# Kernel optimization log

Hardware: AMD Instinct MI355X
Metric: run time of the kernel (lower is better)

## Reference

```python
import jax, jax.numpy as jnp
import numpy as np

B, IN, F, HID, D, RH, OUT, C, R = 4096, 1024, 512, 128, 128, 64, 1, 10, 16


def setup_inputs() -> dict:
    key = jax.random.key(0)
    ks = jax.random.split(key, 24)
    def p(k, shape, s=0.05):
        return jax.random.normal(k, shape, jnp.float32) * s
    return {
        'x': jax.random.normal(ks[0], (B, IN), jnp.float32),
        'pref': jax.random.uniform(ks[1], (R, 2), jnp.float32),
        'base_w': p(ks[2], (F, IN)), 'base_b': p(ks[3], (F,)),
        'wm1_w': p(ks[4], (16, 2)), 'wm1_b': p(ks[5], (16,)),
        'wm2_w': p(ks[6], (C, 16)), 'wm2_b': p(ks[7], (C,)),
        'ray0_w': p(ks[8], (C, RH, 2)), 'ray0_b': p(ks[9], (C, RH)),
        'ray2_w': p(ks[10], (C, D, RH)), 'ray2_b': p(ks[11], (C, D)),
        'fc1_w': p(ks[12], (C, HID * F, D)), 'fc1_b': p(ks[13], (C, HID * F)),
        'b1_w': p(ks[14], (C, HID, D)), 'b1_b': p(ks[15], (C, HID)),
        'fc2_w': p(ks[16], (C, OUT * HID, D)), 'fc2_b': p(ks[17], (C, OUT * HID)),
        'b2_w': p(ks[18], (C, OUT, D)), 'b2_b': p(ks[19], (C, OUT)),
    }


def reference(x, pref, base_w, base_b, wm1_w, wm1_b, wm2_w, wm2_b,
              ray0_w, ray0_b, ray2_w, ray2_b, fc1_w, fc1_b,
              b1_w, b1_b, fc2_w, fc2_b, b2_w, b2_b):
    # base feature extractor: (B, F)
    feature = x @ base_w.T + base_b
    # client mixing weights per ray: (R, C), normalized over clients
    h = jax.nn.relu(pref @ wm1_w.T + wm1_b)
    w = jax.nn.sigmoid(h @ wm2_w.T + wm2_b)
    w = w / jnp.sum(w, axis=1, keepdims=True)
    # merged ray-MLP (nonlinear -> merge the tiny weights explicitly per ray)
    m0w = jnp.einsum('rc,cod->rod', w, ray0_w)          # (R, RH, 2)
    r1 = jax.nn.relu(jnp.einsum('rd,rod->ro', pref, m0w) + w @ ray0_b)
    m2w = jnp.einsum('rc,coh->roh', w, ray2_w)          # (R, D, RH)
    ray2v = jnp.einsum('rh,roh->ro', r1, m2w) + w @ ray2_b  # (R, D)

    def hyper(Wc, bc):
        # sum_c w[r,c] * (ray2v[r] @ Wc[c].T + bc[c])  == F.linear with merged params
        per_client = jnp.einsum('rd,cod->rco', ray2v, Wc)   # (R, C, O)
        return jnp.einsum('rc,rco->ro', w, per_client) + w @ bc

    W1 = hyper(fc1_w, fc1_b).reshape(R, HID, F)   # generated layer-1 weight
    b1 = hyper(b1_w, b1_b)                        # (R, HID)
    W2 = hyper(fc2_w, fc2_b).reshape(R, OUT, HID) # generated layer-2 weight
    b2 = hyper(b2_w, b2_b)                        # (R, OUT)

    v1 = jnp.einsum('bf,rhf->rbh', feature, W1) + b1[:, None, :]  # (R, B, HID)
    out = jnp.einsum('rbh,roh->rbo', v1, W2) + b2[:, None, :]     # (R, B, OUT)
    return jax.nn.sigmoid(out), out
```

## Files before the change

### kernel.cpp

```cpp
#include <hip/hip_runtime.h>
#include <hip/hip_cooperative_groups.h>
#include <cstddef>
#include <cstdint>


#define WS_WT    0
#define WS_RV    160
#define WS_W2T   2208
#define WS_WEFF  4256
#define WS_WFIN  12448
#define WS_BFIN  28832
#define WS_ZERO_BEG WS_RV
#define WS_ZERO_CNT (WS_BFIN + 16 - WS_RV)

namespace cg = cooperative_groups;

__device__ __forceinline__ void front_mlp_flat(const float* __restrict__ pref,
                                               const float* __restrict__ wm1_w,
                                               const float* __restrict__ wm1_b,
                                               const float* __restrict__ wm2_w,
                                               const float* __restrict__ wm2_b,
                                               float* sh1, float* sw, float* sinv) {
  const int t = threadIdx.x;
  {
    int r = t >> 4, j = t & 15;
    float v = pref[r * 2 + 0] * wm1_w[j * 2 + 0] + pref[r * 2 + 1] * wm1_w[j * 2 + 1] + wm1_b[j];
    sh1[r * 16 + j] = fmaxf(v, 0.f);
  }
  __syncthreads();
  if (t < 160) {
    int r = t / 10, c = t % 10;
    float z = wm2_b[c];
    for (int j = 0; j < 16; ++j) z += sh1[r * 16 + j] * wm2_w[c * 16 + j];
    sw[r * 10 + c] = 1.f / (1.f + expf(-z));
  }
  __syncthreads();
  if (t < 16) {
    float s = 0.f;
    for (int c = 0; c < 10; ++c) s += sw[t * 10 + c];
    sinv[t] = 1.f / s;
  }
  __syncthreads();
  if (t < 160) {
    int r = t / 10, c = t % 10;
    sw[r * 10 + c] = sw[r * 10 + c] * sinv[r];
  }
  __syncthreads();
}

__global__ __launch_bounds__(256, 2) void k_all(
    const float* __restrict__ x, const float* __restrict__ pref,
    const float* __restrict__ base_w, const float* __restrict__ base_b,
    const float* __restrict__ wm1_w, const float* __restrict__ wm1_b,
    const float* __restrict__ wm2_w, const float* __restrict__ wm2_b,
    const float* __restrict__ ray0_w, const float* __restrict__ ray0_b,
    const float* __restrict__ ray2_w, const float* __restrict__ ray2_b,
    const float* __restrict__ fc1_w, const float* __restrict__ fc1_b,
    const float* __restrict__ b1_w, const float* __restrict__ b1_b,
    const float* __restrict__ fc2_w, const float* __restrict__ fc2_b,
    const float* __restrict__ b2_w, const float* __restrict__ b2_b,
    float* __restrict__ ws, float* __restrict__ out) {
  __shared__ float4 sm4[4096];
  float* smf = (float*)sm4;
  cg::grid_group grid = cg::this_grid();
  const int t = threadIdx.x;
  const int blk = blockIdx.x;
  const int gid = blk * 256 + t;

  if (gid < 12288) ws[WS_RV + gid] = 0.f;
  else if (gid < 12304) ws[WS_BFIN + (gid - 12288)] = 0.f;
  grid.sync();

  if (blk < 80) {
    float* sh1  = smf;
    float* sw   = smf + 256;
    float* sinv = smf + 416;
    float* r1s  = smf + 432;
    front_mlp_flat(pref, wm1_w, wm1_b, wm2_w, wm2_b, sh1, sw, sinv);
    for (int it = t; it < 1024; it += 256) {
      int r = it >> 6, o = it & 63;
      float m0 = 0.f, m1 = 0.f, rb = 0.f;
      for (int c = 0; c < 10; ++c) {
        float wv = sw[r * 10 + c];
        m0 += wv * ray0_w[(c * 64 + o) * 2 + 0];
        m1 += wv * ray0_w[(c * 64 + o) * 2 + 1];
        rb += wv * ray0_b[c * 64 + o];
      }
      float v = pref[r * 2 + 0] * m0 + pref[r * 2 + 1] * m1 + rb;
      r1s[r * 65 + o] = fmaxf(v, 0.f);
    }
    __syncthreads();
    const int pair = blk * 16 + (t >> 4);
    const int r = t & 15;
    const float* row = ray2_w + (size_t)pair * 64;
    const float* r1r = r1s + r * 65;
    float dot = 0.f;
#pragma unroll
    for (int k = 0; k < 64; ++k) dot += row[k] * r1r[k];
    int c = pair >> 7, d = pair & 127;
    atomicAdd(&ws[WS_RV + r * 128 + d], sw[r * 10 + c] * dot);

    if (blk == 0) {
      if (t < 160) ws[WS_WT + t] = sw[(t & 15) * 10 + (t >> 4)];
      for (int i = t; i < 2048; i += 256) {
        int rr = i >> 7, dd = i & 127;
        float s = 0.f;
        for (int cc = 0; cc < 10; ++cc) s += sw[rr * 10 + cc] * ray2_b[cc * 128 + dd];
        atomicAdd(&ws[WS_RV + i], s);
      }
    } else if (blk == 1) {
      for (int i = t; i < 2048; i += 256) {
        int h = i >> 4, rr = i & 15;
        float s = 0.f;
        for (int cc = 0; cc < 10; ++cc) s += sw[rr * 10 + cc] * fc2_b[cc * 128 + h];
        atomicAdd(&ws[WS_W2T + i], s);
      }
    }
  }
  grid.sync();

  {
    const int wid = t >> 6, lane = t & 63;
    const int rid = blk * 4 + wid;
    if (rid < 1280) {
      float2 rvl[16];
#pragma unroll
      for (int r = 0; r < 16; ++r) rvl[r] = *(const float2*)&ws[WS_RV + r * 128 + lane * 2];
      float2 a = *(const float2*)&fc2_w[(size_t)rid * 128 + lane * 2];
      float u[16];
#pragma unroll
      for (int r = 0; r < 16; ++r) u[r] = a.x * rvl[r].x + a.y * rvl[r].y;
#pragma unroll
      for (int m = 1; m <= 32; m <<= 1) {
#pragma unroll
        for (int r = 0; r < 16; ++r) u[r] += __shfl_xor(u[r], m, 64);
      }
      if (lane == 0) {
        int c = rid >> 7, h = rid & 127;
#pragma unroll
        for (int r = 0; r < 16; ++r)
          atomicAdd(&ws[WS_W2T + h * 16 + r], u[r] * ws[WS_WT + c * 16 + r]);
      }
    }
  }
  grid.sync();

  {
    float* scoef = smf;
    float* bfred = smf + 2560;
    const int wid = t >> 6, lane = t & 63, l32 = lane & 31;
    const int ch0 = (blk >> 6) * 160;
    const int fp  = (blk & 63) * 4 + wid;
    for (int i = t; i < 2560; i += 256) {
      int chl = i >> 4, r = i & 15;
      int ch = ch0 + chl, c = ch >> 7, h = ch & 127;
      scoef[i] = ws[WS_WT + c * 16 + r] * ws[WS_W2T + h * 16 + r];
    }
    float4 rv[16];
#pragma unroll
    for (int r = 0; r < 16; ++r) rv[r] = *(const float4*)&ws[WS_RV + r * 128 + l32 * 4];
    __syncthreads();

    float acc[16];
#pragma unroll
    for (int r = 0; r < 16; ++r) acc[r] = 0.f;

    const float4* p = (const float4*)fc1_w + (size_t)ch0 * 16384 + fp * 64 + lane;
    float4 buf[8];
#pragma unroll
    for (int j = 0; j < 8; ++j) buf[j] = p[(size_t)j * 16384];

    for (int g = 0; g < 20; ++g) {
#pragma unroll
      for (int k = 0; k < 8; ++k) {
        const int chl = g * 8 + k;
        float4 cur = buf[k];
        int nxt = chl + 8; if (nxt > 159) nxt = 159;
        buf[k] = p[(size_t)nxt * 16384];
        const float4* cf = (const float4*)(scoef + chl * 16);
        float4 c0 = cf[0], c1 = cf[1], c2 = cf[2], c3 = cf[3];
        float cw[16] = {c0.x, c0.y, c0.z, c0.w, c1.x, c1.y, c1.z, c1.w,
                        c2.x, c2.y, c2.z, c2.w, c3.x, c3.y, c3.z, c3.w};
#pragma unroll
        for (int r = 0; r < 16; ++r) {
          float tt = cur.x * rv[r].x + cur.y * rv[r].y + cur.z * rv[r].z + cur.w * rv[r].w;
          acc[r] = fmaf(cw[r], tt, acc[r]);
        }
      }
    }
#pragma unroll
    for (int m = 1; m <= 16; m <<= 1) {
#pragma unroll
      for (int r = 0; r < 16; ++r) acc[r] += __shfl_xor(acc[r], m, 64);
    }
    if (l32 == 0) {
      const int f = fp * 2 + (lane >> 5);
#pragma unroll
      for (int r = 0; r < 16; ++r) atomicAdd(&ws[WS_WEFF + r * 512 + f], acc[r]);
    }
    __syncthreads();

    if (blk < 16) {
      const int bb = blk;
      const int f = (bb & 1) * 256 + t;
      const int ch0b = (bb >> 1) * 160;
      for (int i = t; i < 2560; i += 256) {
        int chl = i >> 4, r = i & 15;
        int ch = ch0b + chl, c = ch >> 7, h = ch & 127;
        scoef[i] = ws[WS_WT + c * 16 + r] * ws[WS_W2T + h * 16 + r];
      }
      __syncthreads();
      float a2[16];
#pragma unroll
      for (int r = 0; r < 16; ++r) a2[r] = 0.f;
      const float* q = fc1_b + (size_t)ch0b * 512 + f;
      float b4[4];
#pragma unroll
      for (int j = 0; j < 4; ++j) b4[j] = q[(size_t)j * 512];
      for (int g = 0; g < 40; ++g) {
#pragma unroll
        for (int k = 0; k < 4; ++k) {
          const int it = g * 4 + k;
          float xv = b4[k];
          int nxt = it + 4; if (nxt > 159) nxt = 159;
          b4[k] = q[(size_t)nxt * 512];
          const float4* cf = (const float4*)(scoef + it * 16);
          float4 c0 = cf[0], c1 = cf[1], c2 = cf[2], c3 = cf[3];
          float cw[16] = {c0.x, c0.y, c0.z, c0.w, c1.x, c1.y, c1.z, c1.w,
                          c2.x, c2.y, c2.z, c2.w, c3.x, c3.y, c3.z, c3.w};
#pragma unroll
          for (int r = 0; r < 16; ++r) a2[r] = fmaf(cw[r], xv, a2[r]);
        }
      }
#pragma unroll
      for (int r = 0; r < 16; ++r) atomicAdd(&ws[WS_WEFF + r * 512 + f], a2[r]);
    } else if (blk < 24) {
      const int hb = blk - 16;
      const int ch0b = hb * 160;
      for (int i = t; i < 2560; i += 256) {
        int chl = i >> 4, r = i & 15;
        int ch = ch0b + chl, c = ch >> 7, h = ch & 127;
        scoef[i] = ws[WS_WT + c * 16 + r] * ws[WS_W2T + h * 16 + r];
      }
      __syncthreads();
      float2 rv2[16];
#pragma unroll
      for (int r = 0; r < 16; ++r) rv2[r] = *(const float2*)&ws[WS_RV + r * 128 + lane * 2];
      float a2[16];
#pragma unroll
      for (int r = 0; r < 16; ++r) a2[r] = 0.f;
      const int chl0 = wid * 40;
      const float2* q = (const float2*)b1_w + (size_t)(ch0b + chl0) * 64 + lane;
      float2 b2buf[4];
#pragma unroll
      for (int j = 0; j < 4; ++j) b2buf[j] = q[(size_t)j * 64];
      for (int g = 0; g < 10; ++g) {
#pragma unroll
        for (int k = 0; k < 4; ++k) {
          const int it = g * 4 + k;
          float2 cur = b2buf[k];
          int nxt = it + 4; if (nxt > 39) nxt = 39;
          b2buf[k] = q[(size_t)nxt * 64];
          const float4* cf = (const float4*)(scoef + (chl0 + it) * 16);
          float4 c0 = cf[0], c1 = cf[1], c2 = cf[2], c3 = cf[3];
          float cw[16] = {c0.x, c0.y, c0.z, c0.w, c1.x, c1.y, c1.z, c1.w,
                          c2.x, c2.y, c2.z, c2.w, c3.x, c3.y, c3.z, c3.w};
#pragma unroll
          for (int r = 0; r < 16; ++r)
            a2[r] = fmaf(cw[r], cur.x * rv2[r].x + cur.y * rv2[r].y, a2[r]);
        }
      }
#pragma unroll
      for (int m = 1; m <= 32; m <<= 1) {
#pragma unroll
        for (int r = 0; r < 16; ++r) a2[r] += __shfl_xor(a2[r], m, 64);
      }
      if (lane == 0) {
#pragma unroll
        for (int r = 0; r < 16; ++r) bfred[wid * 16 + r] = a2[r];
      }
      __syncthreads();
      if (t < 16)
        atomicAdd(&ws[WS_BFIN + t], bfred[t] + bfred[16 + t] + bfred[32 + t] + bfred[48 + t]);
    } else if (blk == 24) {
      float a2[16];
#pragma unroll
      for (int r = 0; r < 16; ++r) a2[r] = 0.f;
      for (int i = t; i < 1280; i += 256) {
        int c = i >> 7, h = i & 127;
        float v = b1_b[c * 128 + h];
#pragma unroll
        for (int r = 0; r < 16; ++r)
          a2[r] = fmaf(ws[WS_WT + c * 16 + r] * ws[WS_W2T + h * 16 + r], v, a2[r]);
      }
      for (int i = t; i < 1280; i += 256) {
        int c = i >> 7, d = i & 127;
        float v = b2_w[c * 128 + d];
#pragma unroll
        for (int r = 0; r < 16; ++r)
          a2[r] = fmaf(ws[WS_WT + c * 16 + r] * ws[WS_RV + r * 128 + d], v, a2[r]);
      }
      if (t < 10) {
        float v = b2_b[t];
#pragma unroll
        for (int r = 0; r < 16; ++r) a2[r] = fmaf(ws[WS_WT + t * 16 + r], v, a2[r]);
      }
#pragma unroll
      for (int m = 1; m <= 32; m <<= 1) {
#pragma unroll
        for (int r = 0; r < 16; ++r) a2[r] += __shfl_xor(a2[r], m, 64);
      }
      if (lane == 0) {
#pragma unroll
        for (int r = 0; r < 16; ++r) bfred[wid * 16 + r] = a2[r];
      }
      __syncthreads();
      if (t < 16)
        atomicAdd(&ws[WS_BFIN + t], bfred[t] + bfred[16 + t] + bfred[32 + t] + bfred[48 + t]);
    }
  }
  grid.sync();

  if (blk < 32) {
    const int il = t & 31, fg = t >> 5;
    const int i = blk * 32 + il;
    const float* WEFF = ws + WS_WEFF;
    float a4[16];
#pragma unroll
    for (int r = 0; r < 16; ++r) a4[r] = 0.f;
    const int f0 = fg * 64;
    for (int f = f0; f < f0 + 64; ++f) {
      float bw = base_w[(size_t)f * 1024 + i];
#pragma unroll
      for (int r = 0; r < 16; ++r) a4[r] = fmaf(WEFF[r * 512 + f], bw, a4[r]);
    }
    float* red = smf;
#pragma unroll
    for (int r = 0; r < 16; ++r) red[fg * 512 + il * 16 + r] = a4[r];
    __syncthreads();
    for (int o = t; o < 512; o += 256) {
      int ir = o >> 4, r = o & 15;
      float s = 0.f;
#pragma unroll
      for (int fg2 = 0; fg2 < 8; ++fg2) s += red[fg2 * 512 + ir * 16 + r];
      ws[WS_WFIN + r * 1024 + blk * 32 + ir] = s;
    }
  } else if (blk == 32) {
    if (t < 64) {
      const float* WEFF = ws + WS_WEFF;
      float a2[16];
#pragma unroll
      for (int r = 0; r < 16; ++r) a2[r] = 0.f;
      for (int f = t; f < 512; f += 64) {
        float v = base_b[f];
#pragma unroll
        for (int r = 0; r < 16; ++r) a2[r] = fmaf(WEFF[r * 512 + f], v, a2[r]);
      }
#pragma unroll
      for (int m = 1; m <= 32; m <<= 1) {
#pragma unroll
        for (int r = 0; r < 16; ++r) a2[r] += __shfl_xor(a2[r], m, 64);
      }
      if (t == 0) {
#pragma unroll
        for (int r = 0; r < 16; ++r) atomicAdd(&ws[WS_BFIN + r], a2[r]);
      }
    }
  }
  grid.sync();

  if (blk < 256) {
    float4* wfs = sm4;
    const float4* wf4 = (const float4*)(ws + WS_WFIN);
#pragma unroll
    for (int k = 0; k < 16; ++k) wfs[t + 256 * k] = wf4[t + 256 * k];
    __syncthreads();

    const int b0 = blk * 16;
    const int bp = t >> 5;
    const int isub = t & 31;
    const int bA = b0 + bp * 2;
    const float* xa = x + (size_t)bA * 1024;
    const float* xb = xa + 1024;
    float acc0[16], acc1[16];
#pragma unroll
    for (int r = 0; r < 16; ++r) { acc0[r] = 0.f; acc1[r] = 0.f; }

    for (int chunk = 0; chunk < 4; ++chunk) {
#pragma unroll
      for (int j = 0; j < 2; ++j) {
        const int off = chunk * 256 + j * 128 + isub * 4;
        float4 xv0 = *(const float4*)&xa[off];
        float4 xv1 = *(const float4*)&xb[off];
        const float4* wrow = wfs + chunk * 64 + j * 32 + isub;
#pragma unroll
        for (int r = 0; r < 16; ++r) {
          float4 w = wrow[r * 256];
          acc0[r] += xv0.x * w.x + xv0.y * w.y + xv0.z * w.z + xv0.w * w.w;
          acc1[r] += xv1.x * w.x + xv1.y * w.y + xv1.z * w.z + xv1.w * w.w;
        }
      }
    }
#pragma unroll
    for (int m = 1; m <= 16; m <<= 1) {
#pragma unroll
      for (int r = 0; r < 16; ++r) {
        acc0[r] += __shfl_xor(acc0[r], m, 64);
        acc1[r] += __shfl_xor(acc1[r], m, 64);
      }
    }
    if (isub == 0) {
#pragma unroll
      for (int r = 0; r < 16; ++r) {
        float bf = ws[WS_BFIN + r];
        float v0 = acc0[r] + bf;
        float v1 = acc1[r] + bf;
        out[r * 4096 + bA] = 1.f / (1.f + expf(-v0));
        out[r * 4096 + bA + 1] = 1.f / (1.f + expf(-v1));
        out[65536 + r * 4096 + bA] = v0;
        out[65536 + r * 4096 + bA + 1] = v1;
      }
    }
  }
}

__device__ __forceinline__ void front_mlp(const float* __restrict__ pref,
                                          const float* __restrict__ wm1_w,
                                          const float* __restrict__ wm1_b,
                                          const float* __restrict__ wm2_w,
                                          const float* __restrict__ wm2_b,
                                          float (*sh1)[16], float (*sw)[10],
                                          float* sinv) {
  const int t = threadIdx.x;
  {
    int r = t >> 4, j = t & 15;
    float v = pref[r * 2 + 0] * wm1_w[j * 2 + 0] + pref[r * 2 + 1] * wm1_w[j * 2 + 1] + wm1_b[j];
    sh1[r][j] = fmaxf(v, 0.f);
  }
  __syncthreads();
  if (t < 160) {
    int r = t / 10, c = t % 10;
    float z = wm2_b[c];
    for (int j = 0; j < 16; ++j) z += sh1[r][j] * wm2_w[c * 16 + j];
    sw[r][c] = 1.f / (1.f + expf(-z));
  }
  __syncthreads();
  if (t < 16) {
    float s = 0.f;
    for (int c = 0; c < 10; ++c) s += sw[t][c];
    sinv[t] = 1.f / s;
  }
  __syncthreads();
  if (t < 160) {
    int r = t / 10, c = t % 10;
    sw[r][c] = sw[r][c] * sinv[r];
  }
  __syncthreads();
}

__global__ __launch_bounds__(256) void k_stage1(
    const float* __restrict__ pref, const float* __restrict__ wm1_w,
    const float* __restrict__ wm1_b, const float* __restrict__ wm2_w,
    const float* __restrict__ wm2_b, const float* __restrict__ ray0_w,
    const float* __restrict__ ray0_b, const float* __restrict__ ray2_w,
    const float* __restrict__ ray2_b, const float* __restrict__ fc2_b,
    float* __restrict__ ws) {
  __shared__ float sh1[16][16];
  __shared__ float sw[16][10];
  __shared__ float sinv[16];
  __shared__ float r1s[16][65];
  const int t = threadIdx.x;
  front_mlp(pref, wm1_w, wm1_b, wm2_w, wm2_b, sh1, sw, sinv);
  for (int it = t; it < 1024; it += 256) {
    int r = it >> 6, o = it & 63;
    float m0 = 0.f, m1 = 0.f, rb = 0.f;
    for (int c = 0; c < 10; ++c) {
      float wv = sw[r][c];
      m0 += wv * ray0_w[(c * 64 + o) * 2 + 0];
      m1 += wv * ray0_w[(c * 64 + o) * 2 + 1];
      rb += wv * ray0_b[c * 64 + o];
    }
    float v = pref[r * 2 + 0] * m0 + pref[r * 2 + 1] * m1 + rb;
    r1s[r][o] = fmaxf(v, 0.f);
  }
  __syncthreads();
  const int pair = blockIdx.x * 16 + (t >> 4);
  const int r = t & 15;
  const float* row = ray2_w + (size_t)pair * 64;
  const float* r1r = r1s[r];
  float dot = 0.f;
#pragma unroll
  for (int k = 0; k < 64; ++k) dot += row[k] * r1r[k];
  int c = pair >> 7, d = pair & 127;
  atomicAdd(&ws[WS_RV + r * 128 + d], sw[r][c] * dot);

  if (blockIdx.x == 0) {
    if (t < 160) ws[WS_WT + t] = sw[t & 15][t >> 4];
    for (int i = t; i < 2048; i += 256) {
      int rr = i >> 7, dd = i & 127;
      float s = 0.f;
      for (int cc = 0; cc < 10; ++cc) s += sw[rr][cc] * ray2_b[cc * 128 + dd];
      atomicAdd(&ws[WS_RV + i], s);
    }
  } else if (blockIdx.x == 1) {
    for (int i = t; i < 2048; i += 256) {
      int h = i >> 4, rr = i & 15;
      float s = 0.f;
      for (int cc = 0; cc < 10; ++cc) s += sw[rr][cc] * fc2_b[cc * 128 + h];
      atomicAdd(&ws[WS_W2T + i], s);
    }
  }
}

__global__ __launch_bounds__(256) void k_stage2(const float* __restrict__ fc2_w,
                                                float* __restrict__ ws) {
  const int t = threadIdx.x;
  const int lane = t & 63;
  const int wv = blockIdx.x * 4 + (t >> 6);
  float2 rv2[16];
#pragma unroll
  for (int r = 0; r < 16; ++r) rv2[r] = *(const float2*)&ws[WS_RV + r * 128 + lane * 2];
  for (int q = 0; q < 4; ++q) {
    int rid = wv * 4 + q;
    int c = rid >> 7, h = rid & 127;
    float2 a = *(const float2*)&fc2_w[(size_t)rid * 128 + lane * 2];
    float u[16];
#pragma unroll
    for (int r = 0; r < 16; ++r) u[r] = a.x * rv2[r].x + a.y * rv2[r].y;
#pragma unroll
    for (int m = 1; m <= 32; m <<= 1) {
#pragma unroll
      for (int r = 0; r < 16; ++r) u[r] += __shfl_xor(u[r], m, 64);
    }
    if (lane == 0) {
#pragma unroll
      for (int r = 0; r < 16; ++r)
        atomicAdd(&ws[WS_W2T + h * 16 + r], u[r] * ws[WS_WT + c * 16 + r]);
    }
  }
}

__global__ __launch_bounds__(256, 3) void k_main(
    const float* __restrict__ fc1_w, const float* __restrict__ fc1_b,
    const float* __restrict__ b1_w, const float* __restrict__ b1_b,
    const float* __restrict__ b2_w, const float* __restrict__ b2_b,
    float* __restrict__ ws) {
  __shared__ float scoef[2560];
  __shared__ float bfred[4][16];
  const int blk = blockIdx.x;
  const int t = threadIdx.x;

  if (blk < 2048) {
    const int wid = t >> 6, lane = t & 63, l32 = lane & 31;
    const int ch0 = (blk >> 6) * 40;
    const int fp = (blk & 63) * 4 + wid;
    for (int i = t; i < 640; i += 256) {
      int chl = i >> 4, r = i & 15;
      int ch = ch0 + chl, c = ch >> 7, h = ch & 127;
      scoef[i] = ws[WS_WT + c * 16 + r] * ws[WS_W2T + h * 16 + r];
    }
    float4 rv[16];
#pragma unroll
    for (int r = 0; r < 16; ++r) rv[r] = *(const float4*)&ws[WS_RV + r * 128 + l32 * 4];
    __syncthreads();

    float acc[16];
#pragma unroll
    for (int r = 0; r < 16; ++r) acc[r] = 0.f;

    const float4* p = (const float4*)fc1_w + (size_t)ch0 * 16384 + fp * 64 + lane;

    float4 buf[8];
#pragma unroll
    for (int j = 0; j < 8; ++j) buf[j] = p[(size_t)j * 16384];

    for (int g = 0; g < 5; ++g) {
#pragma unroll
      for (int k = 0; k < 8; ++k) {
        const int chl = g * 8 + k;
        float4 cur = buf[k];
        int nxt = chl + 8; if (nxt > 39) nxt = 39;
        buf[k] = p[(size_t)nxt * 16384];
        const float4* cf = (const float4*)(scoef + chl * 16);
        float4 c0 = cf[0], c1 = cf[1], c2 = cf[2], c3 = cf[3];
        float cw[16] = {c0.x, c0.y, c0.z, c0.w, c1.x, c1.y, c1.z, c1.w,
                        c2.x, c2.y, c2.z, c2.w, c3.x, c3.y, c3.z, c3.w};
#pragma unroll
        for (int r = 0; r < 16; ++r) {
          float tt = cur.x * rv[r].x + cur.y * rv[r].y + cur.z * rv[r].z + cur.w * rv[r].w;
          acc[r] = fmaf(cw[r], tt, acc[r]);
        }
      }
    }

#pragma unroll
    for (int m = 1; m <= 16; m <<= 1) {
#pragma unroll
      for (int r = 0; r < 16; ++r) acc[r] += __shfl_xor(acc[r], m, 64);
    }
    if (l32 == 0) {
      const int f = fp * 2 + (lane >> 5);
#pragma unroll
      for (int r = 0; r < 16; ++r) atomicAdd(&ws[WS_WEFF + r * 512 + f], acc[r]);
    }
  } else if (blk < 2064) {
    const int bb = blk - 2048;
    const int f = (bb & 1) * 256 + t;
    const int ch0 = (bb >> 1) * 160;
    for (int i = t; i < 2560; i += 256) {
      int chl = i >> 4, r = i & 15;
      int ch = ch0 + chl, c = ch >> 7, h = ch & 127;
      scoef[i] = ws[WS_WT + c * 16 + r] * ws[WS_W2T + h * 16 + r];
    }
    __syncthreads();
    float acc[16];
#pragma unroll
    for (int r = 0; r < 16; ++r) acc[r] = 0.f;
    const float* q = fc1_b + (size_t)ch0 * 512 + f;
    float b4[4];
#pragma unroll
    for (int j = 0; j < 4; ++j) b4[j] = q[(size_t)j * 512];
    for (int g = 0; g < 40; ++g) {
#pragma unroll
      for (int k = 0; k < 4; ++k) {
        const int it = g * 4 + k;
        float xv = b4[k];
        int nxt = it + 4; if (nxt > 159) nxt = 159;
        b4[k] = q[(size_t)nxt * 512];
        const float4* cf = (const float4*)(scoef + it * 16);
        float4 c0 = cf[0], c1 = cf[1], c2 = cf[2], c3 = cf[3];
        float cw[16] = {c0.x, c0.y, c0.z, c0.w, c1.x, c1.y, c1.z, c1.w,
                        c2.x, c2.y, c2.z, c2.w, c3.x, c3.y, c3.z, c3.w};
#pragma unroll
        for (int r = 0; r < 16; ++r) acc[r] = fmaf(cw[r], xv, acc[r]);
      }
    }
#pragma unroll
    for (int r = 0; r < 16; ++r) atomicAdd(&ws[WS_WEFF + r * 512 + f], acc[r]);
  } else if (blk < 2072) {
    const int hb = blk - 2064;
    const int wid = t >> 6, lane = t & 63;
    const int ch0b = hb * 160;
    for (int i = t; i < 2560; i += 256) {
      int chl = i >> 4, r = i & 15;
      int ch = ch0b + chl, c = ch >> 7, h = ch & 127;
      scoef[i] = ws[WS_WT + c * 16 + r] * ws[WS_W2T + h * 16 + r];
    }
    __syncthreads();
    float2 rv2[16];
#pragma unroll
    for (int r = 0; r < 16; ++r) rv2[r] = *(const float2*)&ws[WS_RV + r * 128 + lane * 2];
    float acc[16];
#pragma unroll
    for (int r = 0; r < 16; ++r) acc[r] = 0.f;
    const int chl0 = wid * 40;
    const float2* q = (const float2*)b1_w + (size_t)(ch0b + chl0) * 64 + lane;
    float2 b2buf[4];
#pragma unroll
    for (int j = 0; j < 4; ++j) b2buf[j] = q[(size_t)j * 64];
    for (int g = 0; g < 10; ++g) {
#pragma unroll
      for (int k = 0; k < 4; ++k) {
        const int it = g * 4 + k;
        float2 cur = b2buf[k];
        int nxt = it + 4; if (nxt > 39) nxt = 39;
        b2buf[k] = q[(size_t)nxt * 64];
        const float4* cf = (const float4*)(scoef + (chl0 + it) * 16);
        float4 c0 = cf[0], c1 = cf[1], c2 = cf[2], c3 = cf[3];
        float cw[16] = {c0.x, c0.y, c0.z, c0.w, c1.x, c1.y, c1.z, c1.w,
                        c2.x, c2.y, c2.z, c2.w, c3.x, c3.y, c3.z, c3.w};
#pragma unroll
        for (int r = 0; r < 16; ++r)
          acc[r] = fmaf(cw[r], cur.x * rv2[r].x + cur.y * rv2[r].y, acc[r]);
      }
    }
#pragma unroll
    for (int m = 1; m <= 32; m <<= 1) {
#pragma unroll
      for (int r = 0; r < 16; ++r) acc[r] += __shfl_xor(acc[r], m, 64);
    }
    if (lane == 0) {
#pragma unroll
      for (int r = 0; r < 16; ++r) bfred[wid][r] = acc[r];
    }
    __syncthreads();
    if (t < 16)
      atomicAdd(&ws[WS_BFIN + t], bfred[0][t] + bfred[1][t] + bfred[2][t] + bfred[3][t]);
  } else {
    const int wid = t >> 6, lane = t & 63;
    float acc[16];
#pragma unroll
    for (int r = 0; r < 16; ++r) acc[r] = 0.f;
    for (int i = t; i < 1280; i += 256) {
      int c = i >> 7, h = i & 127;
      float v = b1_b[c * 128 + h];
#pragma unroll
      for (int r = 0; r < 16; ++r)
        acc[r] = fmaf(ws[WS_WT + c * 16 + r] * ws[WS_W2T + h * 16 + r], v, acc[r]);
    }
    for (int i = t; i < 1280; i += 256) {
      int c = i >> 7, d = i & 127;
      float v = b2_w[c * 128 + d];
#pragma unroll
      for (int r = 0; r < 16; ++r)
        acc[r] = fmaf(ws[WS_WT + c * 16 + r] * ws[WS_RV + r * 128 + d], v, acc[r]);
    }
    if (t < 10) {
      float v = b2_b[t];
#pragma unroll
      for (int r = 0; r < 16; ++r) acc[r] = fmaf(ws[WS_WT + t * 16 + r], v, acc[r]);
    }
#pragma unroll
    for (int m = 1; m <= 32; m <<= 1) {
#pragma unroll
      for (int r = 0; r < 16; ++r) acc[r] += __shfl_xor(acc[r], m, 64);
    }
    if (lane == 0) {
#pragma unroll
      for (int r = 0; r < 16; ++r) bfred[wid][r] = acc[r];
    }
    __syncthreads();
    if (t < 16)
      atomicAdd(&ws[WS_BFIN + t], bfred[0][t] + bfred[1][t] + bfred[2][t] + bfred[3][t]);
  }
}

__global__ __launch_bounds__(256) void k_wfin(const float* __restrict__ base_w,
                                              const float* __restrict__ base_b,
                                              float* __restrict__ ws) {
  const int t = threadIdx.x;
  const int blk = blockIdx.x;
  const int i = (blk & 3) * 256 + t;
  const int f0 = (blk >> 2) * 16;
  const float* WEFF = ws + WS_WEFF;
  float acc[16];
#pragma unroll
  for (int r = 0; r < 16; ++r) acc[r] = 0.f;
#pragma unroll 4
  for (int f = f0; f < f0 + 16; ++f) {
    float bw = base_w[(size_t)f * 1024 + i];
#pragma unroll
    for (int r = 0; r < 16; ++r) acc[r] = fmaf(WEFF[r * 512 + f], bw, acc[r]);
  }
#pragma unroll
  for (int r = 0; r < 16; ++r) atomicAdd(&ws[WS_WFIN + r * 1024 + i], acc[r]);

  if (blk == 0 && t < 64) {
    float a2[16];
#pragma unroll
    for (int r = 0; r < 16; ++r) a2[r] = 0.f;
    for (int f = t; f < 512; f += 64) {
      float v = base_b[f];
#pragma unroll
      for (int r = 0; r < 16; ++r) a2[r] = fmaf(WEFF[r * 512 + f], v, a2[r]);
    }
#pragma unroll
    for (int m = 1; m <= 32; m <<= 1) {
#pragma unroll
      for (int r = 0; r < 16; ++r) a2[r] += __shfl_xor(a2[r], m, 64);
    }
    if (t == 0) {
#pragma unroll
      for (int r = 0; r < 16; ++r) atomicAdd(&ws[WS_BFIN + r], a2[r]);
    }
  }
}

__global__ __launch_bounds__(256) void k_out(const float* __restrict__ x,
                                             const float* __restrict__ ws,
                                             float* __restrict__ out) {
  __shared__ float4 wfs[4096];
  const int t = threadIdx.x;
  const float4* wf4 = (const float4*)(ws + WS_WFIN);
#pragma unroll
  for (int k = 0; k < 16; ++k) wfs[t + 256 * k] = wf4[t + 256 * k];
  __syncthreads();

  const int b0 = blockIdx.x * 16;
  const int bp = t >> 5;
  const int isub = t & 31;
  const int bA = b0 + bp * 2;
  const float* xa = x + (size_t)bA * 1024;
  const float* xb = xa + 1024;
  float acc0[16], acc1[16];
#pragma unroll
  for (int r = 0; r < 16; ++r) { acc0[r] = 0.f; acc1[r] = 0.f; }

  for (int chunk = 0; chunk < 4; ++chunk) {
#pragma unroll
    for (int j = 0; j < 2; ++j) {
      const int off = chunk * 256 + j * 128 + isub * 4;
      float4 xv0 = *(const float4*)&xa[off];
      float4 xv1 = *(const float4*)&xb[off];
      const float4* wrow = wfs + chunk * 64 + j * 32 + isub;
#pragma unroll
      for (int r = 0; r < 16; ++r) {
        float4 w = wrow[r * 256];
        acc0[r] += xv0.x * w.x + xv0.y * w.y + xv0.z * w.z + xv0.w * w.w;
        acc1[r] += xv1.x * w.x + xv1.y * w.y + xv1.z * w.z + xv1.w * w.w;
      }
    }
  }
#pragma unroll
  for (int m = 1; m <= 16; m <<= 1) {
#pragma unroll
    for (int r = 0; r < 16; ++r) {
      acc0[r] += __shfl_xor(acc0[r], m, 64);
      acc1[r] += __shfl_xor(acc1[r], m, 64);
    }
  }
  if (isub == 0) {
#pragma unroll
    for (int r = 0; r < 16; ++r) {
      float bf = ws[WS_BFIN + r];
      float v0 = acc0[r] + bf;
      float v1 = acc1[r] + bf;
      out[r * 4096 + bA] = 1.f / (1.f + expf(-v0));
      out[r * 4096 + bA + 1] = 1.f / (1.f + expf(-v1));
      out[65536 + r * 4096 + bA] = v0;
      out[65536 + r * 4096 + bA + 1] = v1;
    }
  }
}

extern "C" void kernel_launch(void* const* d_in, const int* in_sizes, int n_in,
                              void* d_out, int out_size, void* d_ws, size_t ws_size,
                              hipStream_t stream) {
  (void)in_sizes; (void)n_in; (void)out_size; (void)ws_size;
  const float* x      = (const float*)d_in[0];
  const float* pref   = (const float*)d_in[1];
  const float* base_w = (const float*)d_in[2];
  const float* base_b = (const float*)d_in[3];
  const float* wm1_w  = (const float*)d_in[4];
  const float* wm1_b  = (const float*)d_in[5];
  const float* wm2_w  = (const float*)d_in[6];
  const float* wm2_b  = (const float*)d_in[7];
  const float* ray0_w = (const float*)d_in[8];
  const float* ray0_b = (const float*)d_in[9];
  const float* ray2_w = (const float*)d_in[10];
  const float* ray2_b = (const float*)d_in[11];
  const float* fc1_w  = (const float*)d_in[12];
  const float* fc1_b  = (const float*)d_in[13];
  const float* b1_w   = (const float*)d_in[14];
  const float* b1_b   = (const float*)d_in[15];
  const float* fc2_w  = (const float*)d_in[16];
  const float* fc2_b  = (const float*)d_in[17];
  const float* b2_w   = (const float*)d_in[18];
  const float* b2_b   = (const float*)d_in[19];
  float* ws  = (float*)d_ws;
  float* out = (float*)d_out;

  static int g_mode = -1;
  if (g_mode < 0) {
    int maxb = 0;
    hipError_t e1 = hipOccupancyMaxActiveBlocksPerMultiprocessor(&maxb, k_all, 256, 0);
    int coop = 0, dev = 0;
    (void)hipGetDevice(&dev);
    hipError_t e2 = hipDeviceGetAttribute(&coop, hipDeviceAttributeCooperativeLaunch, dev);
    g_mode = (e1 == hipSuccess && maxb >= 2 && (e2 != hipSuccess || coop != 0)) ? 1 : 0;
  }

  if (g_mode == 1) {
    void* args[] = {
        (void*)&x, (void*)&pref, (void*)&base_w, (void*)&base_b,
        (void*)&wm1_w, (void*)&wm1_b, (void*)&wm2_w, (void*)&wm2_b,
        (void*)&ray0_w, (void*)&ray0_b, (void*)&ray2_w, (void*)&ray2_b,
        (void*)&fc1_w, (void*)&fc1_b, (void*)&b1_w, (void*)&b1_b,
        (void*)&fc2_w, (void*)&fc2_b, (void*)&b2_w, (void*)&b2_b,
        (void*)&ws, (void*)&out};
    hipError_t e = hipLaunchCooperativeKernel(k_all, dim3(512), dim3(256), args, 0, stream);
    if (e == hipSuccess) return;
    g_mode = 0;
  }

  hipMemsetAsync(ws + WS_ZERO_BEG, 0, (size_t)WS_ZERO_CNT * sizeof(float), stream);
  k_stage1<<<80, 256, 0, stream>>>(pref, wm1_w, wm1_b, wm2_w, wm2_b,
                                   ray0_w, ray0_b, ray2_w, ray2_b, fc2_b, ws);
  k_stage2<<<80, 256, 0, stream>>>(fc2_w, ws);
  k_main<<<2073, 256, 0, stream>>>(fc1_w, fc1_b, b1_w, b1_b, b2_w, b2_b, ws);
  k_wfin<<<128, 256, 0, stream>>>(base_w, base_b, ws);
  k_out<<<256, 256, 0, stream>>>(x, ws, out);
}
```

Baseline: 557.9 us.

## Recompute small ray-MLP stages per block to drop grid syncs and atomics

Every block now redundantly computes the mixing weights, the merged ray vector and the generated layer-2 weights in shared memory. This removes the initial zero-fill pass and two grid-wide barriers along with their atomic accumulations. Per-slice partial sums for the effective weights and the final bias are written to separate workspace slots and reduced by the consumers, so no atomics are needed. The fc1 bias contribution is folded into the main fc1 pass. The cost is redundant per-block compute on fc2_w and ray2_w (each block reads all of fc2_w) and extra partial-sum traffic.

```diff
diff --git a/kernel.cpp b/kernel.cpp
--- a/kernel.cpp
+++ b/kernel.cpp
@@ -3,6 +3,10 @@
 #include <cstddef>
 #include <cstdint>
 
+
+#define WS2_WEFFP 0
+#define WS2_WFIN  65536
+#define WS2_PARTS 81920
 
 #define WS_WT    0
 #define WS_RV    160
@@ -61,22 +65,25 @@
     const float* __restrict__ b2_w, const float* __restrict__ b2_b,
     float* __restrict__ ws, float* __restrict__ out) {
   __shared__ float4 sm4[4096];
+  __shared__ float bfin_s[16];
   float* smf = (float*)sm4;
+  float* sw   = smf;
+  float* sinv = smf + 160;
+  float* sh1  = smf + 176;
+  float* rvl  = smf + 432;
+  float* w2t  = smf + 2544;
+  float* X    = smf + 4720;
+  float* bfred= smf + 8880;
+
   cg::grid_group grid = cg::this_grid();
   const int t = threadIdx.x;
   const int blk = blockIdx.x;
-  const int gid = blk * 256 + t;
-
-  if (gid < 12288) ws[WS_RV + gid] = 0.f;
-  else if (gid < 12304) ws[WS_BFIN + (gid - 12288)] = 0.f;
-  grid.sync();
-
-  if (blk < 80) {
-    float* sh1  = smf;
-    float* sw   = smf + 256;
-    float* sinv = smf + 416;
-    float* r1s  = smf + 432;
-    front_mlp_flat(pref, wm1_w, wm1_b, wm2_w, wm2_b, sh1, sw, sinv);
+  const int wid = t >> 6, lane = t & 63, l32 = lane & 31;
+
+  front_mlp_flat(pref, wm1_w, wm1_b, wm2_w, wm2_b, sh1, sw, sinv);
+
+  {
+    float* r1s = X;
     for (int it = t; it < 1024; it += 256) {
       int r = it >> 6, o = it & 63;
       float m0 = 0.f, m1 = 0.f, rb = 0.f;
@@ -90,86 +97,103 @@
       r1s[r * 65 + o] = fmaxf(v, 0.f);
     }
     __syncthreads();
-    const int pair = blk * 16 + (t >> 4);
-    const int r = t & 15;
-    const float* row = ray2_w + (size_t)pair * 64;
-    const float* r1r = r1s + r * 65;
-    float dot = 0.f;
-#pragma unroll
-    for (int k = 0; k < 64; ++k) dot += row[k] * r1r[k];
-    int c = pair >> 7, d = pair & 127;
-    atomicAdd(&ws[WS_RV + r * 128 + d], sw[r * 10 + c] * dot);
-
-    if (blk == 0) {
-      if (t < 160) ws[WS_WT + t] = sw[(t & 15) * 10 + (t >> 4)];
-      for (int i = t; i < 2048; i += 256) {
-        int rr = i >> 7, dd = i & 127;
-        float s = 0.f;
-        for (int cc = 0; cc < 10; ++cc) s += sw[rr * 10 + cc] * ray2_b[cc * 128 + dd];
-        atomicAdd(&ws[WS_RV + i], s);
-      }
-    } else if (blk == 1) {
-      for (int i = t; i < 2048; i += 256) {
-        int h = i >> 4, rr = i & 15;
-        float s = 0.f;
-        for (int cc = 0; cc < 10; ++cc) s += sw[rr * 10 + cc] * fc2_b[cc * 128 + h];
-        atomicAdd(&ws[WS_W2T + i], s);
-      }
-    }
-  }
-  grid.sync();
+    const int d = t & 127, rh = (t >> 7) * 8;
+    float accv[8];
+#pragma unroll
+    for (int j = 0; j < 8; ++j) accv[j] = 0.f;
+    for (int c = 0; c < 10; ++c) {
+      const float4* row4 = (const float4*)(ray2_w + (size_t)(c * 128 + d) * 64);
+      float dtmp[8];
+#pragma unroll
+      for (int j = 0; j < 8; ++j) dtmp[j] = 0.f;
+#pragma unroll
+      for (int k4 = 0; k4 < 16; ++k4) {
+        float4 rw = row4[k4];
+#pragma unroll
+        for (int rr = 0; rr < 8; ++rr) {
+          const float* rr1 = r1s + (rh + rr) * 65 + k4 * 4;
+          dtmp[rr] += rw.x * rr1[0] + rw.y * rr1[1] + rw.z * rr1[2] + rw.w * rr1[3];
+        }
+      }
+      float rb = ray2_b[c * 128 + d];
+#pragma unroll
+      for (int rr = 0; rr < 8; ++rr)
+        accv[rr] += sw[(rh + rr) * 10 + c] * (dtmp[rr] + rb);
+    }
+#pragma unroll
+    for (int rr = 0; rr < 8; ++rr) rvl[(rh + rr) * 132 + d] = accv[rr];
+  }
+  __syncthreads();
 
   {
-    const int wid = t >> 6, lane = t & 63;
-    const int rid = blk * 4 + wid;
-    if (rid < 1280) {
-      float2 rvl[16];
-#pragma unroll
-      for (int r = 0; r < 16; ++r) rvl[r] = *(const float2*)&ws[WS_RV + r * 128 + lane * 2];
-      float2 a = *(const float2*)&fc2_w[(size_t)rid * 128 + lane * 2];
-      float u[16];
-#pragma unroll
-      for (int r = 0; r < 16; ++r) u[r] = a.x * rvl[r].x + a.y * rvl[r].y;
-#pragma unroll
-      for (int m = 1; m <= 32; m <<= 1) {
-#pragma unroll
-        for (int r = 0; r < 16; ++r) u[r] += __shfl_xor(u[r], m, 64);
-      }
-      if (lane == 0) {
-        int c = rid >> 7, h = rid & 127;
-#pragma unroll
-        for (int r = 0; r < 16; ++r)
-          atomicAdd(&ws[WS_W2T + h * 16 + r], u[r] * ws[WS_WT + c * 16 + r]);
-      }
-    }
-  }
-  grid.sync();
+    float* stg = X;
+    const int hl = t >> 3;
+    const int rg = (t & 7) * 2;
+    float accw[4][2];
+#pragma unroll
+    for (int a = 0; a < 4; ++a) { accw[a][0] = 0.f; accw[a][1] = 0.f; }
+    for (int c = 0; c < 10; ++c) {
+      for (int ch = 0; ch < 4; ++ch) {
+        __syncthreads();
+        const float4* src = (const float4*)(fc2_w + ((size_t)c * 128 + ch * 32) * 128);
+#pragma unroll
+        for (int k = 0; k < 4; ++k) {
+          int j = t + 256 * k;
+          int h_loc = j >> 5, dof = (j & 31) * 4;
+          float4 v = src[j];
+          float* dst = stg + h_loc * 130 + dof;
+          ((float2*)dst)[0] = make_float2(v.x, v.y);
+          ((float2*)dst)[1] = make_float2(v.z, v.w);
+        }
+        __syncthreads();
+        float dt0 = 0.f, dt1 = 0.f;
+        const float2* srow = (const float2*)(stg + hl * 130);
+        const float2* rv0 = (const float2*)(rvl + (rg + 0) * 132);
+        const float2* rv1 = (const float2*)(rvl + (rg + 1) * 132);
+#pragma unroll 8
+        for (int d2 = 0; d2 < 64; ++d2) {
+          float2 fv = srow[d2];
+          float2 a0 = rv0[d2], a1 = rv1[d2];
+          dt0 += fv.x * a0.x + fv.y * a0.y;
+          dt1 += fv.x * a1.x + fv.y * a1.y;
+        }
+        int h = ch * 32 + hl;
+        float fb = fc2_b[c * 128 + h];
+        accw[ch][0] += sw[(rg + 0) * 10 + c] * (dt0 + fb);
+        accw[ch][1] += sw[(rg + 1) * 10 + c] * (dt1 + fb);
+      }
+    }
+#pragma unroll
+    for (int ch = 0; ch < 4; ++ch) {
+      int h = ch * 32 + hl;
+      w2t[h * 17 + rg] = accw[ch][0];
+      w2t[h * 17 + rg + 1] = accw[ch][1];
+    }
+  }
+  __syncthreads();
+
+  float* scoef = X;
+  const int cc = blk >> 6;
+  const int ch0 = cc * 160;
+  const int fp = (blk & 63) * 4 + wid;
+  for (int i = t; i < 2560; i += 256) {
+    int chl = i >> 4, r = i & 15;
+    int ch = ch0 + chl;
+    scoef[i] = sw[r * 10 + (ch >> 7)] * w2t[(ch & 127) * 17 + r];
+  }
+  float4 rv[16];
+#pragma unroll
+  for (int r = 0; r < 16; ++r) rv[r] = *(const float4*)&rvl[r * 132 + l32 * 4];
+  __syncthreads();
 
   {
-    float* scoef = smf;
-    float* bfred = smf + 2560;
-    const int wid = t >> 6, lane = t & 63, l32 = lane & 31;
-    const int ch0 = (blk >> 6) * 160;
-    const int fp  = (blk & 63) * 4 + wid;
-    for (int i = t; i < 2560; i += 256) {
-      int chl = i >> 4, r = i & 15;
-      int ch = ch0 + chl, c = ch >> 7, h = ch & 127;
-      scoef[i] = ws[WS_WT + c * 16 + r] * ws[WS_W2T + h * 16 + r];
-    }
-    float4 rv[16];
-#pragma unroll
-    for (int r = 0; r < 16; ++r) rv[r] = *(const float4*)&ws[WS_RV + r * 128 + l32 * 4];
-    __syncthreads();
-
     float acc[16];
 #pragma unroll
     for (int r = 0; r < 16; ++r) acc[r] = 0.f;
-
     const float4* p = (const float4*)fc1_w + (size_t)ch0 * 16384 + fp * 64 + lane;
     float4 buf[8];
 #pragma unroll
     for (int j = 0; j < 8; ++j) buf[j] = p[(size_t)j * 16384];
-
     for (int g = 0; g < 20; ++g) {
 #pragma unroll
       for (int k = 0; k < 8; ++k) {
@@ -188,143 +212,124 @@
         }
       }
     }
+    const int f = fp * 2 + (lane >> 5);
+#pragma unroll
+    for (int j = 0; j < 5; ++j) {
+      int chl = l32 + j * 32;
+      float fb = fc1_b[(size_t)(ch0 + chl) * 512 + f];
+#pragma unroll
+      for (int r = 0; r < 16; ++r) acc[r] = fmaf(scoef[chl * 16 + r], fb, acc[r]);
+    }
 #pragma unroll
     for (int m = 1; m <= 16; m <<= 1) {
 #pragma unroll
       for (int r = 0; r < 16; ++r) acc[r] += __shfl_xor(acc[r], m, 64);
     }
     if (l32 == 0) {
-      const int f = fp * 2 + (lane >> 5);
-#pragma unroll
-      for (int r = 0; r < 16; ++r) atomicAdd(&ws[WS_WEFF + r * 512 + f], acc[r]);
-    }
-    __syncthreads();
-
-    if (blk < 16) {
-      const int bb = blk;
-      const int f = (bb & 1) * 256 + t;
-      const int ch0b = (bb >> 1) * 160;
-      for (int i = t; i < 2560; i += 256) {
-        int chl = i >> 4, r = i & 15;
-        int ch = ch0b + chl, c = ch >> 7, h = ch & 127;
-        scoef[i] = ws[WS_WT + c * 16 + r] * ws[WS_W2T + h * 16 + r];
-      }
-      __syncthreads();
-      float a2[16];
-#pragma unroll
-      for (int r = 0; r < 16; ++r) a2[r] = 0.f;
-      const float* q = fc1_b + (size_t)ch0b * 512 + f;
-      float b4[4];
-#pragma unroll
-      for (int j = 0; j < 4; ++j) b4[j] = q[(size_t)j * 512];
-      for (int g = 0; g < 40; ++g) {
-#pragma unroll
-        for (int k = 0; k < 4; ++k) {
-          const int it = g * 4 + k;
-          float xv = b4[k];
-          int nxt = it + 4; if (nxt > 159) nxt = 159;
-          b4[k] = q[(size_t)nxt * 512];
-          const float4* cf = (const float4*)(scoef + it * 16);
-          float4 c0 = cf[0], c1 = cf[1], c2 = cf[2], c3 = cf[3];
-          float cw[16] = {c0.x, c0.y, c0.z, c0.w, c1.x, c1.y, c1.z, c1.w,
-                          c2.x, c2.y, c2.z, c2.w, c3.x, c3.y, c3.z, c3.w};
-#pragma unroll
-          for (int r = 0; r < 16; ++r) a2[r] = fmaf(cw[r], xv, a2[r]);
-        }
-      }
-#pragma unroll
-      for (int r = 0; r < 16; ++r) atomicAdd(&ws[WS_WEFF + r * 512 + f], a2[r]);
-    } else if (blk < 24) {
-      const int hb = blk - 16;
-      const int ch0b = hb * 160;
-      for (int i = t; i < 2560; i += 256) {
-        int chl = i >> 4, r = i & 15;
-        int ch = ch0b + chl, c = ch >> 7, h = ch & 127;
-        scoef[i] = ws[WS_WT + c * 16 + r] * ws[WS_W2T + h * 16 + r];
-      }
-      __syncthreads();
-      float2 rv2[16];
-#pragma unroll
-      for (int r = 0; r < 16; ++r) rv2[r] = *(const float2*)&ws[WS_RV + r * 128 + lane * 2];
-      float a2[16];
-#pragma unroll
-      for (int r = 0; r < 16; ++r) a2[r] = 0.f;
-      const int chl0 = wid * 40;
-      const float2* q = (const float2*)b1_w + (size_t)(ch0b + chl0) * 64 + lane;
-      float2 b2buf[4];
-#pragma unroll
-      for (int j = 0; j < 4; ++j) b2buf[j] = q[(size_t)j * 64];
-      for (int g = 0; g < 10; ++g) {
-#pragma unroll
-        for (int k = 0; k < 4; ++k) {
-          const int it = g * 4 + k;
-          float2 cur = b2buf[k];
-          int nxt = it + 4; if (nxt > 39) nxt = 39;
-          b2buf[k] = q[(size_t)nxt * 64];
-          const float4* cf = (const float4*)(scoef + (chl0 + it) * 16);
-          float4 c0 = cf[0], c1 = cf[1], c2 = cf[2], c3 = cf[3];
-          float cw[16] = {c0.x, c0.y, c0.z, c0.w, c1.x, c1.y, c1.z, c1.w,
-                          c2.x, c2.y, c2.z, c2.w, c3.x, c3.y, c3.z, c3.w};
-#pragma unroll
-          for (int r = 0; r < 16; ++r)
-            a2[r] = fmaf(cw[r], cur.x * rv2[r].x + cur.y * rv2[r].y, a2[r]);
-        }
-      }
-#pragma unroll
-      for (int m = 1; m <= 32; m <<= 1) {
-#pragma unroll
-        for (int r = 0; r < 16; ++r) a2[r] += __shfl_xor(a2[r], m, 64);
-      }
-      if (lane == 0) {
-#pragma unroll
-        for (int r = 0; r < 16; ++r) bfred[wid * 16 + r] = a2[r];
-      }
-      __syncthreads();
-      if (t < 16)
-        atomicAdd(&ws[WS_BFIN + t], bfred[t] + bfred[16 + t] + bfred[32 + t] + bfred[48 + t]);
-    } else if (blk == 24) {
-      float a2[16];
-#pragma unroll
-      for (int r = 0; r < 16; ++r) a2[r] = 0.f;
-      for (int i = t; i < 1280; i += 256) {
-        int c = i >> 7, h = i & 127;
-        float v = b1_b[c * 128 + h];
+#pragma unroll
+      for (int r = 0; r < 16; ++r)
+        ws[WS2_WEFFP + cc * 8192 + r * 512 + f] = acc[r];
+    }
+  }
+  __syncthreads();
+
+  if (blk < 8) {
+    const int ch0b = blk * 160;
+    for (int i = t; i < 2560; i += 256) {
+      int chl = i >> 4, r = i & 15;
+      int ch = ch0b + chl;
+      scoef[i] = sw[r * 10 + (ch >> 7)] * w2t[(ch & 127) * 17 + r];
+    }
+    __syncthreads();
+    float2 rv2[16];
+#pragma unroll
+    for (int r = 0; r < 16; ++r) rv2[r] = *(const float2*)&rvl[r * 132 + lane * 2];
+    float a2[16];
+#pragma unroll
+    for (int r = 0; r < 16; ++r) a2[r] = 0.f;
+    const int chl0 = wid * 40;
+    const float2* q = (const float2*)b1_w + (size_t)(ch0b + chl0) * 64 + lane;
+    float2 b2buf[4];
+#pragma unroll
+    for (int j = 0; j < 4; ++j) b2buf[j] = q[(size_t)j * 64];
+    for (int g = 0; g < 10; ++g) {
+#pragma unroll
+      for (int k = 0; k < 4; ++k) {
+        const int it = g * 4 + k;
+        float2 cur = b2buf[k];
+        int nxt = it + 4; if (nxt > 39) nxt = 39;
+        b2buf[k] = q[(size_t)nxt * 64];
+        const float4* cf = (const float4*)(scoef + (chl0 + it) * 16);
+        float4 c0 = cf[0], c1 = cf[1], c2 = cf[2], c3 = cf[3];
+        float cw[16] = {c0.x, c0.y, c0.z, c0.w, c1.x, c1.y, c1.z, c1.w,
+                        c2.x, c2.y, c2.z, c2.w, c3.x, c3.y, c3.z, c3.w};
 #pragma unroll
         for (int r = 0; r < 16; ++r)
-          a2[r] = fmaf(ws[WS_WT + c * 16 + r] * ws[WS_W2T + h * 16 + r], v, a2[r]);
-      }
-      for (int i = t; i < 1280; i += 256) {
-        int c = i >> 7, d = i & 127;
-        float v = b2_w[c * 128 + d];
-#pragma unroll
-        for (int r = 0; r < 16; ++r)
-          a2[r] = fmaf(ws[WS_WT + c * 16 + r] * ws[WS_RV + r * 128 + d], v, a2[r]);
-      }
-      if (t < 10) {
-        float v = b2_b[t];
-#pragma unroll
-        for (int r = 0; r < 16; ++r) a2[r] = fmaf(ws[WS_WT + t * 16 + r], v, a2[r]);
-      }
-#pragma unroll
-      for (int m = 1; m <= 32; m <<= 1) {
-#pragma unroll
-        for (int r = 0; r < 16; ++r) a2[r] += __shfl_xor(a2[r], m, 64);
-      }
-      if (lane == 0) {
-#pragma unroll
-        for (int r = 0; r < 16; ++r) bfred[wid * 16 + r] = a2[r];
-      }
-      __syncthreads();
-      if (t < 16)
-        atomicAdd(&ws[WS_BFIN + t], bfred[t] + bfred[16 + t] + bfred[32 + t] + bfred[48 + t]);
-    }
+          a2[r] = fmaf(cw[r], cur.x * rv2[r].x + cur.y * rv2[r].y, a2[r]);
+      }
+    }
+#pragma unroll
+    for (int m = 1; m <= 32; m <<= 1) {
+#pragma unroll
+      for (int r = 0; r < 16; ++r) a2[r] += __shfl_xor(a2[r], m, 64);
+    }
+    if (lane == 0) {
+#pragma unroll
+      for (int r = 0; r < 16; ++r) bfred[wid * 16 + r] = a2[r];
+    }
+    __syncthreads();
+    if (t < 16)
+      ws[WS2_PARTS + blk * 16 + t] = bfred[t] + bfred[16 + t] + bfred[32 + t] + bfred[48 + t];
+  } else if (blk == 8) {
+    float a2[16];
+#pragma unroll
+    for (int r = 0; r < 16; ++r) a2[r] = 0.f;
+    for (int i = t; i < 1280; i += 256) {
+      int c = i >> 7, h = i & 127;
+      float v = b1_b[c * 128 + h];
+#pragma unroll
+      for (int r = 0; r < 16; ++r)
+        a2[r] = fmaf(sw[r * 10 + c] * w2t[h * 17 + r], v, a2[r]);
+    }
+    for (int i = t; i < 1280; i += 256) {
+      int c = i >> 7, d = i & 127;
+      float v = b2_w[c * 128 + d];
+#pragma unroll
+      for (int r = 0; r < 16; ++r)
+        a2[r] = fmaf(sw[r * 10 + c] * rvl[r * 132 + d], v, a2[r]);
+    }
+    if (t < 10) {
+      float v = b2_b[t];
+#pragma unroll
+      for (int r = 0; r < 16; ++r) a2[r] = fmaf(sw[r * 10 + t], v, a2[r]);
+    }
+#pragma unroll
+    for (int m = 1; m <= 32; m <<= 1) {
+#pragma unroll
+      for (int r = 0; r < 16; ++r) a2[r] += __shfl_xor(a2[r], m, 64);
+    }
+    if (lane == 0) {
+#pragma unroll
+      for (int r = 0; r < 16; ++r) bfred[wid * 16 + r] = a2[r];
+    }
+    __syncthreads();
+    if (t < 16)
+      ws[WS2_PARTS + 8 * 16 + t] = bfred[t] + bfred[16 + t] + bfred[32 + t] + bfred[48 + t];
   }
   grid.sync();
 
   if (blk < 32) {
+    float* weffl = smf;
+    float* red   = smf + 8192;
+    for (int idx = t; idx < 8192; idx += 256) {
+      float s = 0.f;
+#pragma unroll
+      for (int c2 = 0; c2 < 8; ++c2) s += ws[WS2_WEFFP + c2 * 8192 + idx];
+      weffl[idx] = s;
+    }
+    __syncthreads();
     const int il = t & 31, fg = t >> 5;
     const int i = blk * 32 + il;
-    const float* WEFF = ws + WS_WEFF;
     float a4[16];
 #pragma unroll
     for (int r = 0; r < 16; ++r) a4[r] = 0.f;
@@ -332,9 +337,8 @@
     for (int f = f0; f < f0 + 64; ++f) {
       float bw = base_w[(size_t)f * 1024 + i];
 #pragma unroll
-      for (int r = 0; r < 16; ++r) a4[r] = fmaf(WEFF[r * 512 + f], bw, a4[r]);
-    }
-    float* red = smf;
+      for (int r = 0; r < 16; ++r) a4[r] = fmaf(weffl[r * 512 + f], bw, a4[r]);
+    }
 #pragma unroll
     for (int r = 0; r < 16; ++r) red[fg * 512 + il * 16 + r] = a4[r];
     __syncthreads();
@@ -343,18 +347,22 @@
       float s = 0.f;
 #pragma unroll
       for (int fg2 = 0; fg2 < 8; ++fg2) s += red[fg2 * 512 + ir * 16 + r];
-      ws[WS_WFIN + r * 1024 + blk * 32 + ir] = s;
+      ws[WS2_WFIN + r * 1024 + blk * 32 + ir] = s;
     }
   } else if (blk == 32) {
     if (t < 64) {
-      const float* WEFF = ws + WS_WEFF;
       float a2[16];
 #pragma unroll
       for (int r = 0; r < 16; ++r) a2[r] = 0.f;
       for (int f = t; f < 512; f += 64) {
-        float v = base_b[f];
-#pragma unroll
-        for (int r = 0; r < 16; ++r) a2[r] = fmaf(WEFF[r * 512 + f], v, a2[r]);
+        float bb = base_b[f];
+#pragma unroll
+        for (int r = 0; r < 16; ++r) {
+          float s = 0.f;
+#pragma unroll
+          for (int c2 = 0; c2 < 8; ++c2) s += ws[WS2_WEFFP + c2 * 8192 + r * 512 + f];
+          a2[r] = fmaf(s, bb, a2[r]);
+        }
       }
 #pragma unroll
       for (int m = 1; m <= 32; m <<= 1) {
@@ -363,15 +371,21 @@
       }
       if (t == 0) {
 #pragma unroll
-        for (int r = 0; r < 16; ++r) atomicAdd(&ws[WS_BFIN + r], a2[r]);
+        for (int r = 0; r < 16; ++r) ws[WS2_PARTS + 9 * 16 + r] = a2[r];
       }
     }
   }
   grid.sync();
 
   if (blk < 256) {
+    if (t < 16) {
+      float s = 0.f;
+#pragma unroll
+      for (int sl = 0; sl < 10; ++sl) s += ws[WS2_PARTS + sl * 16 + t];
+      bfin_s[t] = s;
+    }
     float4* wfs = sm4;
-    const float4* wf4 = (const float4*)(ws + WS_WFIN);
+    const float4* wf4 = (const float4*)(ws + WS2_WFIN);
 #pragma unroll
     for (int k = 0; k < 16; ++k) wfs[t + 256 * k] = wf4[t + 256 * k];
     __syncthreads();
@@ -412,7 +426,7 @@
     if (isub == 0) {
 #pragma unroll
       for (int r = 0; r < 16; ++r) {
-        float bf = ws[WS_BFIN + r];
+        float bf = bfin_s[r];
         float v0 = acc0[r] + bf;
         float v1 = acc1[r] + bf;
         out[r * 4096 + bA] = 1.f / (1.f + expf(-v0));
```

Result: no change. 558.2 us (+0.1%).
